# Kernel tuning notes

Hardware: AMD Instinct MI355X
Metric: run time of the kernel (lower is better)

Reference implementation:

```python
import jax, jax.numpy as jnp
import numpy as np

D_MODEL = 1024
N_HEAD = 16
HEAD_SIZE = D_MODEL // N_HEAD


def setup_inputs() -> dict:
    key = jax.random.key(0)
    ks = jax.random.split(key, 7)
    B, T, E = 2, 2048, D_MODEL
    scale = 0.02
    return {
        "q": jax.random.normal(ks[0], (B, T, E), dtype=jnp.float32),
        "k": jax.random.normal(ks[1], (B, T, E), dtype=jnp.float32),
        "v": jax.random.normal(ks[2], (B, T, E), dtype=jnp.float32),
        "Wq": jax.random.normal(ks[3], (E, E), dtype=jnp.float32) * scale,
        "Wk": jax.random.normal(ks[4], (E, E), dtype=jnp.float32) * scale,
        "Wv": jax.random.normal(ks[5], (E, E), dtype=jnp.float32) * scale,
        "Wo": jax.random.normal(ks[6], (E, E), dtype=jnp.float32) * scale,
    }


def reference(q, k, v, Wq, Wk, Wv, Wo):
    B, T, E = q.shape
    # torch nn.Linear(bias=False): y = x @ W.T
    qh = (q @ Wq.T).reshape(B, T, N_HEAD, HEAD_SIZE).transpose(0, 2, 1, 3)  # [B,H,T,Dh]
    kh = (k @ Wk.T).reshape(B, T, N_HEAD, HEAD_SIZE).transpose(0, 2, 1, 3)
    vh = (v @ Wv.T).reshape(B, T, N_HEAD, HEAD_SIZE).transpose(0, 2, 1, 3)

    scale = 1.0 / jnp.sqrt(jnp.asarray(HEAD_SIZE, dtype=q.dtype))
    wei = jnp.einsum("bhqd,bhkd->bhqk", qh, kh) * scale  # [B,H,T,T]

    # causal mask (tril): positions j > i set to -inf
    causal = jnp.tril(jnp.ones((T, T), dtype=bool))
    wei = jnp.where(causal, wei, jnp.asarray(-jnp.inf, dtype=wei.dtype))

    attn = jax.nn.softmax(wei, axis=-1)
    out = jnp.einsum("bhqk,bhkd->bhqd", attn, vh)  # [B,H,T,Dh]
    out = out.transpose(0, 2, 1, 3).reshape(B, T, E)
    return out @ Wo.T  # dropout p=0.0 -> identity
```

## Files before the change

### kernel.cpp

```cpp
#include <hip/hip_runtime.h>
#include <hip/hip_bf16.h>
#include <cstddef>
#include <cstdint>

#define B_SZ   2
#define T_SEQ  2048
#define E_DIM  1024
#define N_HEAD 16
#define HEAD   64

typedef unsigned short u16;
typedef unsigned int u32;
using frag8 = __attribute__((ext_vector_type(8))) short;
using f32x4 = __attribute__((ext_vector_type(4))) float;

__device__ inline u16 f2bf(float x) {
    __hip_bfloat16 h = __float2bfloat16(x);
    return *reinterpret_cast<u16*>(&h);
}

__device__ inline void gl2lds16(const void* g, void* l) {
    auto gp = reinterpret_cast<const __attribute__((address_space(1))) unsigned int*>(
        reinterpret_cast<uintptr_t>(g));
    auto lp = reinterpret_cast<__attribute__((address_space(3))) unsigned int*>(
        reinterpret_cast<uintptr_t>(l));
    __builtin_amdgcn_global_load_lds(gp, lp, 16, 0, 0);
}

struct CastArgs {
    const float* src[7];
    u16* dst[7];
    int n[7];
    float scale[7];
};

__global__ __launch_bounds__(256) void cast_f32_bf16(CastArgs a) {
    const int t = blockIdx.y;
    const int i0 = (blockIdx.x * 256 + threadIdx.x) * 8;
    if (i0 >= a.n[t]) return;
    const float sc = a.scale[t];
    const float4 f0 = *(const float4*)(a.src[t] + i0);
    const float4 f1 = *(const float4*)(a.src[t] + i0 + 4);
    union { u16 s[8]; uint4 v; } r;
    r.s[0] = f2bf(f0.x * sc); r.s[1] = f2bf(f0.y * sc);
    r.s[2] = f2bf(f0.z * sc); r.s[3] = f2bf(f0.w * sc);
    r.s[4] = f2bf(f1.x * sc); r.s[5] = f2bf(f1.y * sc);
    r.s[6] = f2bf(f1.z * sc); r.s[7] = f2bf(f1.w * sc);
    *(uint4*)(a.dst[t] + i0) = r.v;
}

__device__ inline void gemm_core(const u16* __restrict__ X,
                                 const u16* __restrict__ W,
                                 void* __restrict__ Yv, int mode,
                                 int bm0, int bn0) {
    __shared__ u16 As[2][64 * 64];
    __shared__ u16 Bs[2][128 * 64];

    const int tid = threadIdx.x;
    const int w = tid >> 6;
    const int lane = tid & 63;
    const int ln = lane & 15;
    const int quad = lane >> 4;
    const int wm = (w & 1) * 32;
    const int wn = (w >> 1) * 64;

    const int l8 = lane >> 3;
    const int g = (lane & 7) ^ l8;

    const u16* Ag = X + (size_t)(bm0 + w * 16 + l8) * 1024 + g * 8;
    const u16* Bg = W + (size_t)(bn0 + w * 32 + l8) * 1024 + g * 8;
    const int al = __builtin_amdgcn_readfirstlane(w * 1024);
    const int bl = __builtin_amdgcn_readfirstlane(w * 2048);

    const f32x4 zf = {0.f, 0.f, 0.f, 0.f};
    f32x4 acc[2][4];
#pragma unroll
    for (int mi = 0; mi < 2; ++mi)
#pragma unroll
        for (int nj = 0; nj < 4; ++nj) acc[mi][nj] = zf;

    const int sw = ln & 7;

    gl2lds16(Ag, &As[0][0] + al);
    gl2lds16(Ag + 8 * 1024, &As[0][0] + al + 512);
#pragma unroll
    for (int it = 0; it < 4; ++it)
        gl2lds16(Bg + (size_t)it * 8 * 1024, &Bs[0][0] + bl + it * 512);

    for (int k0 = 0; k0 < 1024; k0 += 64) {
        const int buf = (k0 >> 6) & 1;
        __syncthreads();

        if (k0 + 64 < 1024) {
            gl2lds16(Ag + k0 + 64, &As[buf ^ 1][0] + al);
            gl2lds16(Ag + 8 * 1024 + k0 + 64, &As[buf ^ 1][0] + al + 512);
#pragma unroll
            for (int it = 0; it < 4; ++it)
                gl2lds16(Bg + (size_t)it * 8 * 1024 + k0 + 64,
                         &Bs[buf ^ 1][0] + bl + it * 512);
        }

        frag8 a[2][2], b[4][2];
#pragma unroll
        for (int kc = 0; kc < 2; ++kc) {
            const int slot = ((kc * 4 + quad) ^ sw) * 8;
#pragma unroll
            for (int mi = 0; mi < 2; ++mi)
                a[mi][kc] = *(const frag8*)(&As[buf][0] + (wm + mi * 16 + ln) * 64 + slot);
#pragma unroll
            for (int nj = 0; nj < 4; ++nj)
                b[nj][kc] = *(const frag8*)(&Bs[buf][0] + (wn + nj * 16 + ln) * 64 + slot);
        }
#pragma unroll
        for (int kc = 0; kc < 2; ++kc)
#pragma unroll
            for (int mi = 0; mi < 2; ++mi)
#pragma unroll
                for (int nj = 0; nj < 4; ++nj)
                    acc[mi][nj] = __builtin_amdgcn_mfma_f32_16x16x32_bf16(
                        a[mi][kc], b[nj][kc], acc[mi][nj], 0, 0, 0);
    }

#pragma unroll
    for (int mi = 0; mi < 2; ++mi)
#pragma unroll
        for (int nj = 0; nj < 4; ++nj)
#pragma unroll
            for (int reg = 0; reg < 4; ++reg) {
                const int m = bm0 + wm + mi * 16 + quad * 4 + reg;
                const int n = bn0 + wn + nj * 16 + ln;
                if (mode == 1) {
                    ((float*)Yv)[(size_t)m * E_DIM + n] = acc[mi][nj][reg];
                } else {
                    const int b_ = m >> 11, t_ = m & (T_SEQ - 1);
                    const int h_ = n >> 6, d_ = n & (HEAD - 1);
                    const size_t idx = (mode == 0)
                        ? (((size_t)(b_ * N_HEAD + h_)) * T_SEQ + t_) * HEAD + d_
                        : (((size_t)(b_ * N_HEAD + h_)) * HEAD + d_) * T_SEQ + t_;
                    ((u16*)Yv)[idx] = f2bf(acc[mi][nj][reg]);
                }
            }
}

struct QkvArgs {
    const u16* X[3];
    const u16* W[3];
    u16* Y[3];
};

__global__ __launch_bounds__(256, 3) void gemm_qkv(QkvArgs a) {
    const int z = blockIdx.z;
    gemm_core(a.X[z], a.W[z], a.Y[z], z == 2 ? 2 : 0,
              blockIdx.x * 64, blockIdx.y * 128);
}

__global__ __launch_bounds__(256, 3) void gemm_out(const u16* __restrict__ X,
                                                   const u16* __restrict__ W,
                                                   float* __restrict__ Y) {
    gemm_core(X, W, Y, 1, blockIdx.x * 64, blockIdx.y * 128);
}

__global__ __launch_bounds__(512, 4) void attn_mfma(const u16* __restrict__ Qh,
                                                    const u16* __restrict__ Kh,
                                                    const u16* __restrict__ Vt_g,
                                                    u16* __restrict__ Aa) {
    __shared__ u16 Ks[2][128 * 64];
    __shared__ u16 Vs[2][64 * 128];

    const int tid = threadIdx.x;
    const int w = tid >> 6;
    const int wq = w & 3;
    const int wk = w >> 2;
    const int lane = tid & 63;
    const int ln = lane & 15;
    const int quad = lane >> 4;

    const int i = blockIdx.x;
    const int half = i >> 8;
    const int r_ = i & 255;
    const int bh = r_ >> 3;
    const int j = r_ & 7;
    const int qt = half ? j : (15 - j);
    const int q0 = qt * 128;
    const int qw = q0 + wq * 32;

    const size_t base = (size_t)bh * T_SEQ * HEAD;
    const u16* Qb = Qh + base;
    const u16* Kb = Kh + base;
    const u16* Vtb = Vt_g + base;

    const int l8 = lane >> 3;
    const int gk = (lane & 7) ^ l8;
    const int l16 = lane >> 4;
    const int c16 = lane & 15;
    const int sls = __builtin_amdgcn_readfirstlane(w * 1024);

    frag8 qf[2][2];
#pragma unroll
    for (int qq = 0; qq < 2; ++qq)
#pragma unroll
        for (int kc = 0; kc < 2; ++kc)
            qf[qq][kc] = *(const frag8*)(Qb + (size_t)(qw + qq * 16 + ln) * HEAD +
                                         kc * 32 + quad * 8);

    const f32x4 zf = {0.f, 0.f, 0.f, 0.f};
    f32x4 o[4][2];
    float rsl[2] = {0.f, 0.f};
#pragma unroll
    for (int dt = 0; dt < 4; ++dt)
#pragma unroll
        for (int qq = 0; qq < 2; ++qq) o[dt][qq] = zf;

    const int ktiles = qt + 1;

#pragma unroll
    for (int it = 0; it < 2; ++it) {
        const int krow = w * 16 + it * 8 + l8;
        gl2lds16(Kb + (size_t)krow * HEAD + gk * 8, &Ks[0][0] + sls + it * 512);
        const int vrow = w * 8 + it * 4 + l16;
        const int gv = c16 ^ (vrow & 7);
        gl2lds16(Vtb + (size_t)vrow * T_SEQ + gv * 8, &Vs[0][0] + sls + it * 512);
    }

    const int sw = ln & 7;
    const int hsel = quad >> 1;
    const int s_lo = ((quad & 1) * 2) * 16 + ln;
    const int s_hi = s_lo + 16;

    for (int kt = 0; kt < ktiles; ++kt) {
        const int k0 = kt << 7;
        const int buf = kt & 1;
        __syncthreads();

        if (kt + 1 < ktiles) {
            const int k1 = k0 + 128;
#pragma unroll
            for (int it = 0; it < 2; ++it) {
                const int krow = w * 16 + it * 8 + l8;
                gl2lds16(Kb + (size_t)(k1 + krow) * HEAD + gk * 8,
                         &Ks[buf ^ 1][0] + sls + it * 512);
                const int vrow = w * 8 + it * 4 + l16;
                const int gv = c16 ^ (vrow & 7);
                gl2lds16(Vtb + (size_t)vrow * T_SEQ + k1 + gv * 8,
                         &Vs[buf ^ 1][0] + sls + it * 512);
            }
        }

        const int kbase = k0 + wk * 64;
        if (kbase <= qw + 31) {
            const bool msk = (kbase + 63 > qw);
            u32 pk[4][2][2];
#pragma unroll
            for (int kk = 0; kk < 4; ++kk) {
                f32x4 st[2] = {zf, zf};
#pragma unroll
                for (int kc = 0; kc < 2; ++kc) {
                    const int slot = ((kc * 4 + quad) ^ sw) * 8;
                    const frag8 kf = *(const frag8*)(&Ks[buf][0] +
                                                     (wk * 64 + kk * 16 + ln) * 64 + slot);
                    st[0] = __builtin_amdgcn_mfma_f32_16x16x32_bf16(kf, qf[0][kc], st[0], 0, 0, 0);
                    st[1] = __builtin_amdgcn_mfma_f32_16x16x32_bf16(kf, qf[1][kc], st[1], 0, 0, 0);
                }
#pragma unroll
                for (int qq = 0; qq < 2; ++qq) {
                    float e[4];
#pragma unroll
                    for (int reg = 0; reg < 4; ++reg) {
                        const int key = kbase + kk * 16 + quad * 4 + reg;
                        const int qg = qw + qq * 16 + ln;
                        float ev = __expf(st[qq][reg]);
                        if (msk) ev = (key <= qg) ? ev : 0.f;
                        e[reg] = ev;
                        rsl[qq] += ev;
                    }
                    pk[kk][qq][0] = ((u32)f2bf(e[1]) << 16) | f2bf(e[0]);
                    pk[kk][qq][1] = ((u32)f2bf(e[3]) << 16) | f2bf(e[2]);
                }
            }

#pragma unroll
            for (int kc = 0; kc < 2; ++kc) {
                union { frag8 f; u32 d[4]; } pb[2];
#pragma unroll
                for (int qq = 0; qq < 2; ++qq) {
                    const u32 a00 = __shfl(pk[kc * 2][qq][0], s_lo, 64);
                    const u32 a01 = __shfl(pk[kc * 2][qq][1], s_lo, 64);
                    const u32 a02 = __shfl(pk[kc * 2][qq][0], s_hi, 64);
                    const u32 a03 = __shfl(pk[kc * 2][qq][1], s_hi, 64);
                    const u32 a10 = __shfl(pk[kc * 2 + 1][qq][0], s_lo, 64);
                    const u32 a11 = __shfl(pk[kc * 2 + 1][qq][1], s_lo, 64);
                    const u32 a12 = __shfl(pk[kc * 2 + 1][qq][0], s_hi, 64);
                    const u32 a13 = __shfl(pk[kc * 2 + 1][qq][1], s_hi, 64);
                    pb[qq].d[0] = hsel ? a10 : a00;
                    pb[qq].d[1] = hsel ? a11 : a01;
                    pb[qq].d[2] = hsel ? a12 : a02;
                    pb[qq].d[3] = hsel ? a13 : a03;
                }
                const int slotv = (((wk * 2 + kc) * 4 + quad) ^ sw) * 8;
#pragma unroll
                for (int dt = 0; dt < 4; ++dt) {
                    const frag8 vf = *(const frag8*)(&Vs[buf][0] + (dt * 16 + ln) * 128 + slotv);
                    o[dt][0] = __builtin_amdgcn_mfma_f32_16x16x32_bf16(vf, pb[0].f, o[dt][0], 0, 0, 0);
                    o[dt][1] = __builtin_amdgcn_mfma_f32_16x16x32_bf16(vf, pb[1].f, o[dt][1], 0, 0, 0);
                }
            }
        }
    }

#pragma unroll
    for (int qq = 0; qq < 2; ++qq) {
        rsl[qq] += __shfl_xor(rsl[qq], 16, 64);
        rsl[qq] += __shfl_xor(rsl[qq], 32, 64);
    }

    __syncthreads();
    float* ored = (float*)&Ks[0][0];
    float* lred = (float*)&Vs[0][0];
    if (wk == 1) {
#pragma unroll
        for (int dt = 0; dt < 4; ++dt)
#pragma unroll
            for (int qq = 0; qq < 2; ++qq)
#pragma unroll
                for (int rg = 0; rg < 4; ++rg)
                    ored[(dt * 8 + qq * 4 + rg) * 256 + wq * 64 + lane] = o[dt][qq][rg];
        lred[wq * 64 + lane] = rsl[0];
        lred[256 + wq * 64 + lane] = rsl[1];
    }
    __syncthreads();
    if (wk == 0) {
#pragma unroll
        for (int dt = 0; dt < 4; ++dt)
#pragma unroll
            for (int qq = 0; qq < 2; ++qq)
#pragma unroll
                for (int rg = 0; rg < 4; ++rg)
                    o[dt][qq][rg] += ored[(dt * 8 + qq * 4 + rg) * 256 + wq * 64 + lane];
        rsl[0] += lred[wq * 64 + lane];
        rsl[1] += lred[256 + wq * 64 + lane];

        const float inv0 = 1.f / rsl[0];
        const float inv1 = 1.f / rsl[1];
        const int b_ = bh >> 4, h_ = bh & (N_HEAD - 1);
#pragma unroll
        for (int qq = 0; qq < 2; ++qq) {
            const float inv = qq ? inv1 : inv0;
            const int qg = qw + qq * 16 + ln;
            u16* rowp = Aa + ((size_t)(b_ * T_SEQ + qg)) * E_DIM + h_ * HEAD;
#pragma unroll
            for (int dt = 0; dt < 4; ++dt)
#pragma unroll
                for (int rp = 0; rp < 2; ++rp) {
                    const u32 v = ((u32)f2bf(o[dt][qq][2 * rp + 1] * inv) << 16) |
                                  f2bf(o[dt][qq][2 * rp] * inv);
                    *(u32*)(rowp + dt * 16 + quad * 4 + rp * 2) = v;
                }
        }
    }
}

extern "C" void kernel_launch(void* const* d_in, const int* in_sizes, int n_in,
                              void* d_out, int out_size, void* d_ws, size_t ws_size,
                              hipStream_t stream) {
    const float* q  = (const float*)d_in[0];
    const float* k  = (const float*)d_in[1];
    const float* v  = (const float*)d_in[2];
    const float* Wq = (const float*)d_in[3];
    const float* Wk = (const float*)d_in[4];
    const float* Wv = (const float*)d_in[5];
    const float* Wo = (const float*)d_in[6];

    u16* ws = (u16*)d_ws;
    const size_t M4 = (size_t)4 * 1024 * 1024;
    const size_t M1 = (size_t)1024 * 1024;
    u16* qb  = ws;
    u16* kb  = ws + M4;
    u16* vb  = ws + 2 * M4;
    u16* Wqb = ws + 3 * M4;
    u16* Wkb = ws + 3 * M4 + M1;
    u16* Wvb = ws + 3 * M4 + 2 * M1;
    u16* Wob = ws + 3 * M4 + 3 * M1;
    u16* Qh  = ws + 4 * M4;
    u16* Kh  = ws + 5 * M4;
    u16* Vht = ws + 6 * M4;
    u16* Aa  = ws + 7 * M4;

    CastArgs ca;
    ca.src[0] = q;  ca.src[1] = k;  ca.src[2] = v;
    ca.src[3] = Wq; ca.src[4] = Wk; ca.src[5] = Wv; ca.src[6] = Wo;
    ca.dst[0] = qb;  ca.dst[1] = kb;  ca.dst[2] = vb;
    ca.dst[3] = Wqb; ca.dst[4] = Wkb; ca.dst[5] = Wvb; ca.dst[6] = Wob;
    ca.n[0] = ca.n[1] = ca.n[2] = (int)M4;
    ca.n[3] = ca.n[4] = ca.n[5] = ca.n[6] = (int)M1;
    ca.scale[0] = ca.scale[1] = ca.scale[2] = 1.f;
    ca.scale[3] = 0.125f;
    ca.scale[4] = ca.scale[5] = ca.scale[6] = 1.f;
    cast_f32_bf16<<<dim3(2048, 7), 256, 0, stream>>>(ca);

    QkvArgs ga;
    ga.X[0] = qb;  ga.X[1] = kb;  ga.X[2] = vb;
    ga.W[0] = Wqb; ga.W[1] = Wkb; ga.W[2] = Wvb;
    ga.Y[0] = Qh;  ga.Y[1] = Kh;  ga.Y[2] = Vht;
    gemm_qkv<<<dim3(64, 8, 3), 256, 0, stream>>>(ga);

    attn_mfma<<<dim3(512), 512, 0, stream>>>(Qh, Kh, Vht, Aa);

    gemm_out<<<dim3(64, 8), 256, 0, stream>>>(Aa, Wob, (float*)d_out);
}
```

Baseline: 198.6 us.

## Replace GEMMs with 256x256-tile 4-stage pipelined kernel using dynamic LDS

Replaces the 64x128-tile double-buffered GEMM with a 256x256 tile per 512-thread block, which loads 32-wide K slices into a 4-slot LDS ring through async global-to-LDS copies and explicit vmcnt waits. Each wave now computes 128x64 outputs, which raises MFMA reuse per LDS load. It uses s_setprio around the MFMA burst. The fused QKV launch becomes three separate launches of 64 blocks each, so each GEMM fills only 64 of the chip's CUs. That low occupancy and the loss of concurrency across the three projections may cost more than the reuse saves.

Measured after the change: 290.7 us. 1.46x slower.

```diff
diff --git a/kernel.cpp b/kernel.cpp
--- a/kernel.cpp
+++ b/kernel.cpp
@@ -49,80 +49,88 @@
     *(uint4*)(a.dst[t] + i0) = r.v;
 }
 
-__device__ inline void gemm_core(const u16* __restrict__ X,
-                                 const u16* __restrict__ W,
-                                 void* __restrict__ Yv, int mode,
-                                 int bm0, int bn0) {
-    __shared__ u16 As[2][64 * 64];
-    __shared__ u16 Bs[2][128 * 64];
+__global__ __launch_bounds__(512, 1) void gemm256(const u16* __restrict__ X,
+                                                  const u16* __restrict__ W,
+                                                  void* __restrict__ Yv, int mode) {
+    extern __shared__ u16 sm[];
+    u16* As = sm;
+    u16* Bs = sm + 4 * 8192;
 
     const int tid = threadIdx.x;
     const int w = tid >> 6;
     const int lane = tid & 63;
     const int ln = lane & 15;
     const int quad = lane >> 4;
-    const int wm = (w & 1) * 32;
+    const int wm = (w & 1) * 128;
     const int wn = (w >> 1) * 64;
-
-    const int l8 = lane >> 3;
-    const int g = (lane & 7) ^ l8;
-
-    const u16* Ag = X + (size_t)(bm0 + w * 16 + l8) * 1024 + g * 8;
-    const u16* Bg = W + (size_t)(bn0 + w * 32 + l8) * 1024 + g * 8;
-    const int al = __builtin_amdgcn_readfirstlane(w * 1024);
-    const int bl = __builtin_amdgcn_readfirstlane(w * 2048);
+    const int bm0 = blockIdx.x * 256;
+    const int bn0 = blockIdx.y * 256;
+
+    const int r4 = lane >> 2;
+    const int gch = (lane & 3) ^ (r4 & 3);
+    const int sdst = __builtin_amdgcn_readfirstlane(w * 1024);
+    const int xk = (quad ^ (ln & 3)) * 8;
 
     const f32x4 zf = {0.f, 0.f, 0.f, 0.f};
-    f32x4 acc[2][4];
-#pragma unroll
-    for (int mi = 0; mi < 2; ++mi)
+    f32x4 acc[8][4];
+#pragma unroll
+    for (int mi = 0; mi < 8; ++mi)
 #pragma unroll
         for (int nj = 0; nj < 4; ++nj) acc[mi][nj] = zf;
 
-    const int sw = ln & 7;
-
-    gl2lds16(Ag, &As[0][0] + al);
-    gl2lds16(Ag + 8 * 1024, &As[0][0] + al + 512);
-#pragma unroll
-    for (int it = 0; it < 4; ++it)
-        gl2lds16(Bg + (size_t)it * 8 * 1024, &Bs[0][0] + bl + it * 512);
-
-    for (int k0 = 0; k0 < 1024; k0 += 64) {
-        const int buf = (k0 >> 6) & 1;
-        __syncthreads();
-
-        if (k0 + 64 < 1024) {
-            gl2lds16(Ag + k0 + 64, &As[buf ^ 1][0] + al);
-            gl2lds16(Ag + 8 * 1024 + k0 + 64, &As[buf ^ 1][0] + al + 512);
-#pragma unroll
-            for (int it = 0; it < 4; ++it)
-                gl2lds16(Bg + (size_t)it * 8 * 1024 + k0 + 64,
-                         &Bs[buf ^ 1][0] + bl + it * 512);
+    auto stage = [&](int hh) {
+        const int slot = hh & 3;
+        const int col = hh * 32 + gch * 8;
+#pragma unroll
+        for (int i = 0; i < 2; ++i) {
+            gl2lds16(X + (size_t)(bm0 + w * 32 + i * 16 + r4) * 1024 + col,
+                     As + slot * 8192 + sdst + i * 512);
+            gl2lds16(W + (size_t)(bn0 + w * 32 + i * 16 + r4) * 1024 + col,
+                     Bs + slot * 8192 + sdst + i * 512);
         }
-
-        frag8 a[2][2], b[4][2];
-#pragma unroll
-        for (int kc = 0; kc < 2; ++kc) {
-            const int slot = ((kc * 4 + quad) ^ sw) * 8;
-#pragma unroll
-            for (int mi = 0; mi < 2; ++mi)
-                a[mi][kc] = *(const frag8*)(&As[buf][0] + (wm + mi * 16 + ln) * 64 + slot);
+    };
+
+    stage(0); stage(1); stage(2);
+    asm volatile("s_waitcnt vmcnt(8)" ::: "memory");
+    __builtin_amdgcn_s_barrier();
+    asm volatile("" ::: "memory");
+
+#pragma unroll 4
+    for (int h = 0; h < 32; ++h) {
+        const int slot = h & 3;
+        const u16* sA = As + slot * 8192;
+        const u16* sB = Bs + slot * 8192;
+
+        frag8 a[8], b[4];
+#pragma unroll
+        for (int mi = 0; mi < 8; ++mi)
+            a[mi] = *(const frag8*)(sA + (wm + mi * 16 + ln) * 32 + xk);
+#pragma unroll
+        for (int nj = 0; nj < 4; ++nj)
+            b[nj] = *(const frag8*)(sB + (wn + nj * 16 + ln) * 32 + xk);
+
+        if (h + 3 < 32) stage(h + 3);
+
+        if (h <= 28)      asm volatile("s_waitcnt vmcnt(8)" ::: "memory");
+        else if (h == 29) asm volatile("s_waitcnt vmcnt(4)" ::: "memory");
+        else if (h == 30) asm volatile("s_waitcnt vmcnt(0)" ::: "memory");
+
+        __builtin_amdgcn_s_setprio(1);
+#pragma unroll
+        for (int mi = 0; mi < 8; ++mi)
 #pragma unroll
             for (int nj = 0; nj < 4; ++nj)
-                b[nj][kc] = *(const frag8*)(&Bs[buf][0] + (wn + nj * 16 + ln) * 64 + slot);
-        }
-#pragma unroll
-        for (int kc = 0; kc < 2; ++kc)
-#pragma unroll
-            for (int mi = 0; mi < 2; ++mi)
-#pragma unroll
-                for (int nj = 0; nj < 4; ++nj)
-                    acc[mi][nj] = __builtin_amdgcn_mfma_f32_16x16x32_bf16(
-                        a[mi][kc], b[nj][kc], acc[mi][nj], 0, 0, 0);
-    }
-
-#pragma unroll
-    for (int mi = 0; mi < 2; ++mi)
+                acc[mi][nj] = __builtin_amdgcn_mfma_f32_16x16x32_bf16(
+                    a[mi], b[nj], acc[mi][nj], 0, 0, 0);
+        __builtin_amdgcn_s_setprio(0);
+
+        asm volatile("" ::: "memory");
+        __builtin_amdgcn_s_barrier();
+        asm volatile("" ::: "memory");
+    }
+
+#pragma unroll
+    for (int mi = 0; mi < 8; ++mi)
 #pragma unroll
         for (int nj = 0; nj < 4; ++nj)
 #pragma unroll
@@ -148,17 +156,13 @@
     u16* Y[3];
 };
 
-__global__ __launch_bounds__(256, 3) void gemm_qkv(QkvArgs a) {
+__global__ __launch_bounds__(512, 1) void gemm_qkv(QkvArgs a) {
     const int z = blockIdx.z;
-    gemm_core(a.X[z], a.W[z], a.Y[z], z == 2 ? 2 : 0,
-              blockIdx.x * 64, blockIdx.y * 128);
-}
-
-__global__ __launch_bounds__(256, 3) void gemm_out(const u16* __restrict__ X,
-                                                   const u16* __restrict__ W,
-                                                   float* __restrict__ Y) {
-    gemm_core(X, W, Y, 1, blockIdx.x * 64, blockIdx.y * 128);
-}
+    (void)a; (void)z;
+}
+
+__global__ __launch_bounds__(512, 1) void gemm256_qkv(QkvArgs a);
+
 
 __global__ __launch_bounds__(512, 4) void attn_mfma(const u16* __restrict__ Qh,
                                                     const u16* __restrict__ Kh,
@@ -397,13 +401,14 @@
     ca.scale[4] = ca.scale[5] = ca.scale[6] = 1.f;
     cast_f32_bf16<<<dim3(2048, 7), 256, 0, stream>>>(ca);
 
-    QkvArgs ga;
-    ga.X[0] = qb;  ga.X[1] = kb;  ga.X[2] = vb;
-    ga.W[0] = Wqb; ga.W[1] = Wkb; ga.W[2] = Wvb;
-    ga.Y[0] = Qh;  ga.Y[1] = Kh;  ga.Y[2] = Vht;
-    gemm_qkv<<<dim3(64, 8, 3), 256, 0, stream>>>(ga);
+    (void)hipFuncSetAttribute((const void*)gemm256,
+                              hipFuncAttributeMaxDynamicSharedMemorySize, 131072);
+
+    gemm256<<<dim3(16, 4), 512, 131072, stream>>>(qb, Wqb, Qh, 0);
+    gemm256<<<dim3(16, 4), 512, 131072, stream>>>(kb, Wkb, Kh, 0);
+    gemm256<<<dim3(16, 4), 512, 131072, stream>>>(vb, Wvb, Vht, 2);
 
     attn_mfma<<<dim3(512), 512, 0, stream>>>(Qh, Kh, Vht, Aa);
 
-    gemm_out<<<dim3(64, 8), 256, 0, stream>>>(Aa, Wob, (float*)d_out);
-}
+    gemm256<<<dim3(16, 4), 512, 131072, stream>>>(Aa, Wob, (float*)d_out, 1);
+}
```
